# Kernel tuning notes

Measured on AMD Instinct MI355X. Metric: run time of the kernel, lower is better.

Reference implementation:

```python
import jax, jax.numpy as jnp
import numpy as np

B, L, WD = 4096, 30, 300          # batch of news, title length, word dim
H, AD = 20, 20                    # attention heads, per-head dim
MD = H * AD                       # multi_dim = 400
E, ED = 10, 100                   # entities per news, entity dim
QD = 200                          # query_vector_dim
CAT, CD = 18, 50                  # category vocab / dim
SUB, SD = 300, 50                 # subcategory vocab / dim


def _mha(x, wq, bq, wk, bk, wv, bv):
    # x: [B, L, Din] -> [B, L, MD]; standard multi-head self-attention
    b, l, _ = x.shape
    q = (x @ wq + bq).reshape(b, l, H, AD)
    k = (x @ wk + bk).reshape(b, l, H, AD)
    v = (x @ wv + bv).reshape(b, l, H, AD)
    scores = jnp.einsum('blhd,bmhd->bhlm', q, k) / jnp.sqrt(jnp.asarray(AD, x.dtype))
    attn = jax.nn.softmax(scores, axis=-1)
    out = jnp.einsum('bhlm,bmhd->blhd', attn, v)
    return out.reshape(b, l, MD)


def _layernorm(x, g, b):
    mu = jnp.mean(x, axis=-1, keepdims=True)
    var = jnp.var(x, axis=-1, keepdims=True)
    return (x - mu) / jnp.sqrt(var + 1e-5) * g + b


def _additive(x, w, b, q):
    # x: [B, L, D] -> [B, D]
    scores = jnp.tanh(x @ w + b) @ q            # [B, L]
    alpha = jax.nn.softmax(scores, axis=-1)
    return jnp.einsum('bl,bld->bd', alpha, x)


def setup_inputs() -> dict:
    key = jax.random.key(0)
    ks = iter(jax.random.split(key, 40))
    n = lambda shape, s=0.02: (jax.random.normal(next(ks), shape, dtype=jnp.float32) * s)
    inp = {
        'word_embedding': jax.random.normal(next(ks), (B, L, WD), dtype=jnp.float32),
        'entity_embedding': jax.random.normal(next(ks), (B, E, ED), dtype=jnp.float32),
        'category_index': jax.random.randint(next(ks), (B,), 0, CAT, dtype=jnp.int64 if jax.config.jax_enable_x64 else jnp.int32),
        'subcategory_index': jax.random.randint(next(ks), (B,), 0, SUB, dtype=jnp.int64 if jax.config.jax_enable_x64 else jnp.int32),
        # category / subcategory branches
        'emb_cat': n((CAT, CD), 1.0), 'fc1_w': n((CD, MD)), 'fc1_b': jnp.zeros((MD,), jnp.float32),
        'emb_sub': n((SUB, SD), 1.0), 'fc2_w': n((SD, MD)), 'fc2_b': jnp.zeros((MD,), jnp.float32),
        # word multi-head self-attention
        'wq': n((WD, MD)), 'bq': jnp.zeros((MD,), jnp.float32),
        'wk': n((WD, MD)), 'bk': jnp.zeros((MD,), jnp.float32),
        'wv': n((WD, MD)), 'bv': jnp.zeros((MD,), jnp.float32),
        # shared LayerNorm
        'ln_g': jnp.ones((MD,), jnp.float32), 'ln_b': jnp.zeros((MD,), jnp.float32),
        # word additive attention
        'wa_w': n((MD, QD)), 'wa_b': jnp.zeros((QD,), jnp.float32), 'wa_q': n((QD,), 1.0),
        # entity branch: fc3 + GCN (learnable adjacency over the E entities of a news)
        'fc3_w': n((ED, ED)), 'fc3_b': jnp.zeros((ED,), jnp.float32),
        'gcn_A': n((E, E), 1.0), 'gcn_w': n((ED, MD)), 'gcn_b': jnp.zeros((MD,), jnp.float32),
        'ea_w': n((MD, QD)), 'ea_b': jnp.zeros((QD,), jnp.float32), 'ea_q': n((QD,), 1.0),
        # final news-level additive attention over 4 views
        'na_w': n((MD, QD)), 'na_b': jnp.zeros((QD,), jnp.float32), 'na_q': n((QD,), 1.0),
    }
    return inp


def reference(word_embedding, entity_embedding, category_index, subcategory_index,
              emb_cat, fc1_w, fc1_b, emb_sub, fc2_w, fc2_b,
              wq, bq, wk, bk, wv, bv, ln_g, ln_b,
              wa_w, wa_b, wa_q, fc3_w, fc3_b, gcn_A, gcn_w, gcn_b,
              ea_w, ea_b, ea_q, na_w, na_b, na_q):
    # category / subcategory reps (dropout is identity in eval)
    cat_rep = jnp.tanh(emb_cat[category_index] @ fc1_w + fc1_b)      # [B, MD]
    sub_rep = jnp.tanh(emb_sub[subcategory_index] @ fc2_w + fc2_b)   # [B, MD]
    # word branch
    w = _mha(word_embedding, wq, bq, wk, bk, wv, bv)                 # [B, L, MD]
    w = _layernorm(w, ln_g, ln_b)
    word_rep = jnp.tanh(_additive(w, wa_w, wa_b, wa_q))              # [B, MD]
    # entity branch: fc3 -> intra-news GCN -> shared LayerNorm
    e = jnp.tanh(entity_embedding @ fc3_w + fc3_b)                   # [B, E, ED]
    e = jax.nn.relu(jnp.einsum('ef,bfd->bed', gcn_A, e) @ gcn_w + gcn_b)  # [B, E, MD]
    e = _layernorm(e, ln_g, ln_b)
    ent_rep = jnp.tanh(_additive(e, ea_w, ea_b, ea_q))               # [B, MD]
    # fuse the 4 views with additive attention
    views = jnp.stack([word_rep, ent_rep, cat_rep, sub_rep], axis=1)  # [B, 4, MD]
    news_rep = jnp.tanh(_additive(views, na_w, na_b, na_q))          # [B, MD]
    return news_rep
```

## Files before the change

kernel.cpp:

```cpp
#include <hip/hip_runtime.h>
#include <hip/hip_bf16.h>
#include <math.h>

#define B_  4096
#define L_  30
#define WD_ 300
#define H_  20
#define AD_ 20
#define MD_ 400
#define E_  10
#define ED_ 100
#define QD_ 200
#define CD_ 50
#define SD_ 50

typedef unsigned short ushort_t;
typedef __attribute__((ext_vector_type(8))) short bf16x8_t;
typedef __attribute__((ext_vector_type(4))) float f32x4_t;

#define SX_STR   328
#define QKV_STR  1218
#define OUTB_STR 424
#define SOUT_STR 401
#define P_STR    40
#define WT_K     320
#define WAT_K    416

#define N_WT    (1200 * WT_K)
#define N_WAT   (208 * WAT_K)
#define N_FC3T  (112 * 128)
#define N_GCNT  (400 * 128)
#define N_EAT   (208 * WAT_K)

union FragU {
  unsigned  u[4];
  short     s[8];
  bf16x8_t  h;
};

__device__ __forceinline__ ushort_t f2bf(float f) {
  unsigned u = __builtin_bit_cast(unsigned, f);
  unsigned r = (u + 0x7fffu + ((u >> 16) & 1u)) >> 16;
  return (ushort_t)r;
}
__device__ __forceinline__ float bf2f(ushort_t h) {
  return __builtin_bit_cast(float, ((unsigned)h) << 16);
}
__device__ __forceinline__ float wave_reduce_sum(float v) {
  #pragma unroll
  for (int off = 32; off > 0; off >>= 1) v += __shfl_xor(v, off);
  return v;
}
__device__ __forceinline__ void split2(float v, ushort_t* __restrict__ H,
                                       ushort_t* __restrict__ Lo, int idx) {
  const ushort_t h = f2bf(v);
  H[idx] = h;
  Lo[idx] = f2bf(v - bf2f(h));
}

__global__ __launch_bounds__(256) void prep_weights(
    const float* __restrict__ wq, const float* __restrict__ wk, const float* __restrict__ wv,
    const float* __restrict__ wa_w, const float* __restrict__ fc3_w,
    const float* __restrict__ gcn_w, const float* __restrict__ ea_w,
    ushort_t* __restrict__ Wt, ushort_t* __restrict__ Wat,
    ushort_t* __restrict__ fc3TH, ushort_t* __restrict__ fc3TL,
    ushort_t* __restrict__ gcnTH, ushort_t* __restrict__ gcnTL,
    ushort_t* __restrict__ eaTH, ushort_t* __restrict__ eaTL)
{
  int idx = blockIdx.x * 256 + threadIdx.x;
  if (idx < N_WT) {
    const int n = idx / WT_K, k = idx - n * WT_K;
    float v = 0.f;
    if (k < WD_) {
      const float* w = (n < 400) ? wq : (n < 800) ? wk : wv;
      const int c = (n < 400) ? n : (n < 800) ? n - 400 : n - 800;
      v = w[k * MD_ + c];
    }
    Wt[idx] = f2bf(v);
    return;
  }
  idx -= N_WT;
  if (idx < N_WAT) {
    const int q = idx / WAT_K, d = idx - q * WAT_K;
    Wat[idx] = (q < QD_ && d < MD_) ? f2bf(wa_w[d * QD_ + q]) : (ushort_t)0;
    return;
  }
  idx -= N_WAT;
  if (idx < N_FC3T) {
    const int n = idx / 128, k = idx - n * 128;
    const float v = (n < ED_ && k < ED_) ? fc3_w[k * ED_ + n] : 0.f;
    split2(v, fc3TH, fc3TL, idx);
    return;
  }
  idx -= N_FC3T;
  if (idx < N_GCNT) {
    const int n = idx / 128, k = idx - n * 128;
    const float v = (k < ED_) ? gcn_w[k * MD_ + n] : 0.f;
    split2(v, gcnTH, gcnTL, idx);
    return;
  }
  idx -= N_GCNT;
  if (idx < N_EAT) {
    const int q = idx / WAT_K, d = idx - q * WAT_K;
    const float v = (q < QD_ && d < MD_) ? ea_w[d * QD_ + q] : 0.f;
    split2(v, eaTH, eaTL, idx);
  }
}

__global__ __launch_bounds__(1024, 4) void word_branch_kernel(
    const float* __restrict__ X,
    const ushort_t* __restrict__ Wt, const ushort_t* __restrict__ Wat,
    const float* __restrict__ bq, const float* __restrict__ bk, const float* __restrict__ bv,
    const float* __restrict__ ln_g, const float* __restrict__ ln_b,
    const float* __restrict__ wa_b, const float* __restrict__ wa_q,
    float* __restrict__ word_rep)
{
  __shared__ __align__(16) union {
    ushort_t x[32 * SX_STR];
    ushort_t p[16 * 16 * P_STR];
  } uA;
  __shared__ __align__(16) union {
    ushort_t qkv[30 * QKV_STR];
    ushort_t o[32 * OUTB_STR];
  } uB;
  __shared__ __align__(16) float sOut[30 * SOUT_STR];
  __shared__ float sSc[32];
  __shared__ float sAlpha[32];

  const int b    = blockIdx.x;
  const int tid  = threadIdx.x;
  const int wave = tid >> 6;
  const int lane = tid & 63;
  const int lr   = lane & 15;
  const int kg   = lane >> 4;

  const float* xb = X + (size_t)b * (L_ * WD_);
  {
    const int r = tid >> 5;
    const int c0 = tid & 31;
    #pragma unroll
    for (int k = 0; k < 10; ++k) {
      const int c = c0 + k * 32;
      const float v = (r < L_ && c < WD_) ? xb[r * WD_ + c] : 0.f;
      uA.x[r * SX_STR + c] = f2bf(v);
    }
  }
  if (tid < 32) sSc[tid] = 0.f;
  __syncthreads();

  bf16x8_t axl[10], axh[10];
  #pragma unroll
  for (int ks = 0; ks < 10; ++ks) {
    axl[ks] = *reinterpret_cast<const bf16x8_t*>(&uA.x[lr * SX_STR + ks * 32 + kg * 8]);
    axh[ks] = *reinterpret_cast<const bf16x8_t*>(&uA.x[(16 + lr) * SX_STR + ks * 32 + kg * 8]);
  }
  for (int nt = wave; nt < 75; nt += 16) {
    const ushort_t* wbase = &Wt[(nt * 16 + lr) * WT_K + kg * 8];
    f32x4_t acc0 = {0,0,0,0}, acc1 = {0,0,0,0};
    #pragma unroll
    for (int ks = 0; ks < 10; ++ks) {
      bf16x8_t bf = *reinterpret_cast<const bf16x8_t*>(wbase + ks * 32);
      acc0 = __builtin_amdgcn_mfma_f32_16x16x32_bf16(axl[ks], bf, acc0, 0, 0, 0);
      acc1 = __builtin_amdgcn_mfma_f32_16x16x32_bf16(axh[ks], bf, acc1, 0, 0, 0);
    }
    const int col = nt * 16 + lr;
    const float bias = (col < 400) ? bq[col] : (col < 800) ? bk[col - 400] : bv[col - 800];
    #pragma unroll
    for (int i = 0; i < 4; ++i) {
      uB.qkv[(kg * 4 + i) * QKV_STR + col] = f2bf(acc0[i] + bias);
      const int r2 = 16 + kg * 4 + i;
      if (r2 < L_) uB.qkv[r2 * QKV_STR + col] = f2bf(acc1[i] + bias);
    }
  }
  __syncthreads();

  ushort_t* pw = &uA.p[wave * (16 * P_STR)];
  for (int u = wave; u < 2 * H_; u += 16) {
    const int h = u >> 1, mt = u & 1;
    const int hq = h * AD_, hk = 400 + h * AD_, hv = 800 + h * AD_;

    bf16x8_t aq, bkf[2];
    {
      FragU fq;
      fq.u[0]=fq.u[1]=fq.u[2]=fq.u[3]=0;
      const bool okrow = (mt == 0) || (lr < 14);
      if (okrow && kg < 3) {
        const ushort_t* pq = &uB.qkv[(mt * 16 + lr) * QKV_STR + hq + kg * 8];
        fq.u[0] = *(const unsigned*)(pq);     fq.u[1] = *(const unsigned*)(pq + 2);
        if (kg < 2) { fq.u[2] = *(const unsigned*)(pq + 4); fq.u[3] = *(const unsigned*)(pq + 6); }
      }
      aq = fq.h;
    }
    #pragma unroll
    for (int t = 0; t < 2; ++t) {
      FragU fk;
      fk.u[0]=fk.u[1]=fk.u[2]=fk.u[3]=0;
      const bool okrow = (t == 0) || (lr < 14);
      if (okrow && kg < 3) {
        const ushort_t* pk = &uB.qkv[(t * 16 + lr) * QKV_STR + hk + kg * 8];
        fk.u[0] = *(const unsigned*)(pk);     fk.u[1] = *(const unsigned*)(pk + 2);
        if (kg < 2) { fk.u[2] = *(const unsigned*)(pk + 4); fk.u[3] = *(const unsigned*)(pk + 6); }
      }
      bkf[t] = fk.h;
    }
    f32x4_t c0 = {0,0,0,0}, c1 = {0,0,0,0};
    c0 = __builtin_amdgcn_mfma_f32_16x16x32_bf16(aq, bkf[0], c0, 0, 0, 0);
    c1 = __builtin_amdgcn_mfma_f32_16x16x32_bf16(aq, bkf[1], c1, 0, 0, 0);

    const float SCALE = 0.2236067977499790f;
    #pragma unroll
    for (int i = 0; i < 4; ++i) {
      const float v0 = c0[i] * SCALE;
      const float v1 = (lr < 14) ? c1[i] * SCALE : -1e30f;
      float mx = fmaxf(v0, v1);
      mx = fmaxf(mx, __shfl_xor(mx, 1));
      mx = fmaxf(mx, __shfl_xor(mx, 2));
      mx = fmaxf(mx, __shfl_xor(mx, 4));
      mx = fmaxf(mx, __shfl_xor(mx, 8));
      const float e0 = __expf(v0 - mx);
      const float e1 = (lr < 14) ? __expf(v1 - mx) : 0.f;
      float s = e0 + e1;
      s += __shfl_xor(s, 1);
      s += __shfl_xor(s, 2);
      s += __shfl_xor(s, 4);
      s += __shfl_xor(s, 8);
      const float inv = 1.f / s;
      const int row = kg * 4 + i;
      pw[row * P_STR + lr]      = f2bf(e0 * inv);
      pw[row * P_STR + 16 + lr] = f2bf(e1 * inv);
    }
    __asm__ volatile("s_waitcnt lgkmcnt(0)" ::: "memory");

    bf16x8_t ap = *reinterpret_cast<const bf16x8_t*>(&pw[lr * P_STR + kg * 8]);
    bf16x8_t bvf[2];
    #pragma unroll
    for (int nt = 0; nt < 2; ++nt) {
      FragU f;
      const int d = nt * 16 + lr;
      if (d < AD_) {
        #pragma unroll
        for (int j = 0; j < 8; ++j) {
          const int rm = kg * 8 + j;
          f.s[j] = (rm < L_) ? (short)uB.qkv[rm * QKV_STR + hv + d] : (short)0;
        }
      } else {
        f.u[0]=f.u[1]=f.u[2]=f.u[3]=0;
      }
      bvf[nt] = f.h;
    }
    f32x4_t o0 = {0,0,0,0}, o1 = {0,0,0,0};
    o0 = __builtin_amdgcn_mfma_f32_16x16x32_bf16(ap, bvf[0], o0, 0, 0, 0);
    o1 = __builtin_amdgcn_mfma_f32_16x16x32_bf16(ap, bvf[1], o1, 0, 0, 0);

    #pragma unroll
    for (int nt = 0; nt < 2; ++nt) {
      const f32x4_t o = nt ? o1 : o0;
      const int d = nt * 16 + lr;
      if (d < AD_) {
        #pragma unroll
        for (int i = 0; i < 4; ++i) {
          const int r = mt * 16 + kg * 4 + i;
          if (r < L_) sOut[r * SOUT_STR + h * AD_ + d] = o[i];
        }
      }
    }
  }
  __syncthreads();

  for (int r = wave; r < L_; r += 16) {
    float s = 0.f, s2 = 0.f;
    for (int d = lane; d < MD_; d += 64) { const float v = sOut[r * SOUT_STR + d]; s += v; s2 += v * v; }
    s  = wave_reduce_sum(s);
    s2 = wave_reduce_sum(s2);
    const float mu  = s * (1.f / MD_);
    const float var = s2 * (1.f / MD_) - mu * mu;
    const float inv = rsqrtf(var + 1e-5f);
    for (int d = lane; d < MD_; d += 64) {
      const float nv = (sOut[r * SOUT_STR + d] - mu) * inv * ln_g[d] + ln_b[d];
      sOut[r * SOUT_STR + d] = nv;
      uB.o[r * OUTB_STR + d] = f2bf(nv);
    }
  }
  if (tid < 2 * 416) {
    const int r = 30 + (tid / 416), c = tid - (tid / 416) * 416;
    uB.o[r * OUTB_STR + c] = 0;
  }
  {
    const int id = tid;
    if (id < 30 * 16) {
      const int r = id >> 4, c = 400 + (id & 15);
      uB.o[r * OUTB_STR + c] = 0;
    }
  }
  __syncthreads();

  for (int t = wave; t < 26; t += 16) {
    const int mt = t & 1, nt = t >> 1;
    bf16x8_t afa[13];
    #pragma unroll
    for (int ks = 0; ks < 13; ++ks)
      afa[ks] = *reinterpret_cast<const bf16x8_t*>(&uB.o[(mt * 16 + lr) * OUTB_STR + ks * 32 + kg * 8]);
    const ushort_t* wbase = &Wat[(nt * 16 + lr) * WAT_K + kg * 8];
    f32x4_t acc = {0,0,0,0};
    #pragma unroll
    for (int ks = 0; ks < 13; ++ks) {
      bf16x8_t wf = *reinterpret_cast<const bf16x8_t*>(wbase + ks * 32);
      acc = __builtin_amdgcn_mfma_f32_16x16x32_bf16(afa[ks], wf, acc, 0, 0, 0);
    }
    const int q = nt * 16 + lr;
    if (q < QD_) {
      const float bb = wa_b[q], qq = wa_q[q];
      #pragma unroll
      for (int i = 0; i < 4; ++i) {
        const int row = mt * 16 + kg * 4 + i;
        if (row < L_) atomicAdd(&sSc[row], tanhf(acc[i] + bb) * qq);
      }
    }
  }
  __syncthreads();

  if (wave == 0) {
    const float v = (lane < L_) ? sSc[lane] : -1e30f;
    float mx = v;
    #pragma unroll
    for (int off = 32; off > 0; off >>= 1) mx = fmaxf(mx, __shfl_xor(mx, off));
    const float e = (lane < L_) ? __expf(v - mx) : 0.f;
    float s = e;
    #pragma unroll
    for (int off = 32; off > 0; off >>= 1) s += __shfl_xor(s, off);
    if (lane < L_) sAlpha[lane] = e / s;
  }
  __syncthreads();

  if (tid < MD_) {
    const int d = tid;
    float acc = 0.f;
    #pragma unroll 6
    for (int l = 0; l < L_; ++l) acc += sAlpha[l] * sOut[l * SOUT_STR + d];
    word_rep[(size_t)b * MD_ + d] = tanhf(acc);
  }
}

__global__ __launch_bounds__(512, 4) void entity_branch_kernel(
    const float* __restrict__ Ein,
    const ushort_t* __restrict__ fc3TH, const ushort_t* __restrict__ fc3TL,
    const float* __restrict__ fc3_b,
    const float* __restrict__ gcn_A,
    const ushort_t* __restrict__ gcnTH, const ushort_t* __restrict__ gcnTL,
    const float* __restrict__ gcn_b,
    const float* __restrict__ ln_g, const float* __restrict__ ln_b,
    const ushort_t* __restrict__ eaTH, const ushort_t* __restrict__ eaTL,
    const float* __restrict__ ea_b, const float* __restrict__ ea_q,
    float* __restrict__ ent_rep)
{
  __shared__ __align__(16) ushort_t sEh[16 * 136], sEl[16 * 136];
  __shared__ __align__(16) float    eF[E_ * 104];
  __shared__ __align__(16) ushort_t gH[16 * 136], gL[16 * 136];
  __shared__ __align__(16) float    sR[16 * SOUT_STR];
  __shared__ __align__(16) ushort_t oH[16 * OUTB_STR], oL[16 * OUTB_STR];
  __shared__ float sSc[16];
  __shared__ float sAlpha[16];

  const int b    = blockIdx.x;
  const int tid  = threadIdx.x;
  const int wave = tid >> 6;
  const int lane = tid & 63;
  const int lr   = lane & 15;
  const int kg   = lane >> 4;

  for (int id = tid; id < 16 * 128; id += 512) {
    const int r = id >> 7, c = id & 127;
    const float v = (r < E_ && c < ED_) ? Ein[(size_t)b * (E_ * ED_) + r * ED_ + c] : 0.f;
    const ushort_t hh = f2bf(v);
    sEh[r * 136 + c] = hh;
    sEl[r * 136 + c] = f2bf(v - bf2f(hh));
  }
  for (int id = tid; id < 16 * 136; id += 512) { gH[id] = 0; gL[id] = 0; }
  for (int id = tid; id < 16 * OUTB_STR; id += 512) { oH[id] = 0; oL[id] = 0; }
  if (tid < 16) sSc[tid] = 0.f;
  __syncthreads();

  for (int nt = wave; nt < 7; nt += 8) {
    f32x4_t acc = {0,0,0,0};
    #pragma unroll
    for (int ks = 0; ks < 4; ++ks) {
      const int kb = ks * 32 + kg * 8;
      bf16x8_t ah = *reinterpret_cast<const bf16x8_t*>(&sEh[lr * 136 + kb]);
      bf16x8_t al = *reinterpret_cast<const bf16x8_t*>(&sEl[lr * 136 + kb]);
      bf16x8_t wh = *reinterpret_cast<const bf16x8_t*>(&fc3TH[(nt * 16 + lr) * 128 + kb]);
      bf16x8_t wl = *reinterpret_cast<const bf16x8_t*>(&fc3TL[(nt * 16 + lr) * 128 + kb]);
      acc = __builtin_amdgcn_mfma_f32_16x16x32_bf16(ah, wh, acc, 0, 0, 0);
      acc = __builtin_amdgcn_mfma_f32_16x16x32_bf16(al, wh, acc, 0, 0, 0);
      acc = __builtin_amdgcn_mfma_f32_16x16x32_bf16(ah, wl, acc, 0, 0, 0);
    }
    const int d = nt * 16 + lr;
    if (d < ED_) {
      const float bias = fc3_b[d];
      #pragma unroll
      for (int i = 0; i < 4; ++i) {
        const int r = kg * 4 + i;
        if (r < E_) eF[r * 104 + d] = tanhf(acc[i] + bias);
      }
    }
  }
  __syncthreads();

  for (int id = tid; id < E_ * ED_; id += 512) {
    const int i = id / ED_, d = id - (id / ED_) * ED_;
    float acc = 0.f;
    #pragma unroll
    for (int f = 0; f < E_; ++f) acc += gcn_A[i * E_ + f] * eF[f * 104 + d];
    const ushort_t hh = f2bf(acc);
    gH[i * 136 + d] = hh;
    gL[i * 136 + d] = f2bf(acc - bf2f(hh));
  }
  __syncthreads();

  for (int nt = wave; nt < 25; nt += 8) {
    f32x4_t acc = {0,0,0,0};
    #pragma unroll
    for (int ks = 0; ks < 4; ++ks) {
      const int kb = ks * 32 + kg * 8;
// ... 119 lines not shown
  const int b = blockIdx.x, tid = threadIdx.x;
  for (int d = tid; d < MD_; d += 256) {
    sViews[0][d] = word_rep[(size_t)b * MD_ + d];
    sViews[1][d] = ent_rep[(size_t)b * MD_ + d];
    sViews[2][d] = cat_rep[(size_t)b * MD_ + d];
    sViews[3][d] = sub_rep[(size_t)b * MD_ + d];
  }
  if (tid < 4) sSc[tid] = 0.f;
  __syncthreads();
  for (int id = tid; id < 4 * QD_; id += 256) {
    const int v = id / QD_, q = id - (id / QD_) * QD_;
    float acc = na_b[q];
    #pragma unroll 4
    for (int d = 0; d < MD_; ++d) acc += sViews[v][d] * na_w[d * QD_ + q];
    atomicAdd(&sSc[v], tanhf(acc) * na_q[q]);
  }
  __syncthreads();
  if (tid == 0) {
    float mx = -1e30f;
    for (int v = 0; v < 4; ++v) mx = fmaxf(mx, sSc[v]);
    float sum = 0.f;
    for (int v = 0; v < 4; ++v) { const float e = __expf(sSc[v] - mx); sAlpha[v] = e; sum += e; }
    const float inv = 1.f / sum;
    for (int v = 0; v < 4; ++v) sAlpha[v] *= inv;
  }
  __syncthreads();
  for (int d = tid; d < MD_; d += 256) {
    const float acc = sAlpha[0] * sViews[0][d] + sAlpha[1] * sViews[1][d] +
                      sAlpha[2] * sViews[2][d] + sAlpha[3] * sViews[3][d];
    out[(size_t)b * MD_ + d] = tanhf(acc);
  }
}

extern "C" void kernel_launch(void* const* d_in, const int* in_sizes, int n_in,
                              void* d_out, int out_size, void* d_ws, size_t ws_size,
                              hipStream_t stream) {
  const float* X        = (const float*)d_in[0];
  const float* Ein      = (const float*)d_in[1];
  const int*   cat_idx  = (const int*)d_in[2];
  const int*   sub_idx  = (const int*)d_in[3];
  const float* emb_cat  = (const float*)d_in[4];
  const float* fc1_w    = (const float*)d_in[5];
  const float* fc1_b    = (const float*)d_in[6];
  const float* emb_sub  = (const float*)d_in[7];
  const float* fc2_w    = (const float*)d_in[8];
  const float* fc2_b    = (const float*)d_in[9];
  const float* wq       = (const float*)d_in[10];
  const float* bq       = (const float*)d_in[11];
  const float* wk       = (const float*)d_in[12];
  const float* bk       = (const float*)d_in[13];
  const float* wv       = (const float*)d_in[14];
  const float* bv       = (const float*)d_in[15];
  const float* ln_g     = (const float*)d_in[16];
  const float* ln_b     = (const float*)d_in[17];
  const float* wa_w     = (const float*)d_in[18];
  const float* wa_b     = (const float*)d_in[19];
  const float* wa_q     = (const float*)d_in[20];
  const float* fc3_w    = (const float*)d_in[21];
  const float* fc3_b    = (const float*)d_in[22];
  const float* gcn_A    = (const float*)d_in[23];
  const float* gcn_w    = (const float*)d_in[24];
  const float* gcn_b    = (const float*)d_in[25];
  const float* ea_w     = (const float*)d_in[26];
  const float* ea_b     = (const float*)d_in[27];
  const float* ea_q     = (const float*)d_in[28];
  const float* na_w     = (const float*)d_in[29];
  const float* na_b     = (const float*)d_in[30];
  const float* na_q     = (const float*)d_in[31];

  float* out = (float*)d_out;
  const size_t BM = (size_t)B_ * MD_;
  float* word_rep = (float*)d_ws;
  float* ent_rep  = word_rep + BM;
  float* cat_rep  = ent_rep + BM;
  float* sub_rep  = cat_rep + BM;
  ushort_t* Wt    = (ushort_t*)(sub_rep + BM);
  ushort_t* Wat   = Wt + N_WT;
  ushort_t* fc3TH = Wat + N_WAT;
  ushort_t* fc3TL = fc3TH + N_FC3T;
  ushort_t* gcnTH = fc3TL + N_FC3T;
  ushort_t* gcnTL = gcnTH + N_GCNT;
  ushort_t* eaTH  = gcnTL + N_GCNT;
  ushort_t* eaTL  = eaTH + N_EAT;

  {
    const int total = N_WT + N_WAT + N_FC3T + N_GCNT + N_EAT;
    prep_weights<<<(total + 255) / 256, 256, 0, stream>>>(
        wq, wk, wv, wa_w, fc3_w, gcn_w, ea_w,
        Wt, Wat, fc3TH, fc3TL, gcnTH, gcnTL, eaTH, eaTL);
  }
  word_branch_kernel<<<B_, 1024, 0, stream>>>(X, Wt, Wat, bq, bk, bv,
                                              ln_g, ln_b, wa_b, wa_q, word_rep);
  entity_branch_kernel<<<B_, 512, 0, stream>>>(Ein, fc3TH, fc3TL, fc3_b, gcn_A,
                                               gcnTH, gcnTL, gcn_b,
                                               ln_g, ln_b, eaTH, eaTL, ea_b, ea_q, ent_rep);
  catsub_kernel<<<(2 * B_ * MD_) / 256, 256, 0, stream>>>(cat_idx, sub_idx,
                                                          emb_cat, fc1_w, fc1_b,
                                                          emb_sub, fc2_w, fc2_b,
                                                          cat_rep, sub_rep);
  fuse_kernel<<<B_, 256, 0, stream>>>(word_rep, ent_rep, cat_rep, sub_rep,
                                      na_w, na_b, na_q, out);
}
```

Before: 1.312 ms.

## Make word-branch kernel persistent with half-width QKV staging and global MHA scratch

The word-branch kernel now runs as 512 persistent blocks of 512 threads, each looping over 8 news items instead of one 1024-thread block per item. QKV is computed and consumed in two passes of 10 heads each, so the shared staging buffer is halved. The fp32 attention output moves from shared memory to a per-block global scratch buffer. Together these cut shared-memory and thread footprint per block to raise residency, at the cost of extra global/L2 traffic for the MHA output and more barriers per item.

Result: slower. 1.448 ms (+10.3%).

```diff
diff --git a/kernel.cpp b/kernel.cpp
--- a/kernel.cpp
+++ b/kernel.cpp
@@ -18,13 +18,16 @@
 typedef __attribute__((ext_vector_type(8))) short bf16x8_t;
 typedef __attribute__((ext_vector_type(4))) float f32x4_t;
 
-#define SX_STR   328
-#define QKV_STR  1218
-#define OUTB_STR 424
-#define SOUT_STR 401
-#define P_STR    40
-#define WT_K     320
-#define WAT_K    416
+#define SX_STR    328
+#define QKVH_STR  626
+#define OUTB_STR  424
+#define SOUT_STR  401
+#define P_STR     40
+#define WT_K      320
+#define WAT_K     416
+
+#define WBLK      512
+#define ITERS     (B_ / WBLK)
 
 #define N_WT    (1200 * WT_K)
 #define N_WAT   (208 * WAT_K)
@@ -107,237 +110,262 @@
   }
 }
 
-__global__ __launch_bounds__(1024, 4) void word_branch_kernel(
+__global__ __launch_bounds__(512, 4) void word_branch_kernel(
     const float* __restrict__ X,
     const ushort_t* __restrict__ Wt, const ushort_t* __restrict__ Wat,
     const float* __restrict__ bq, const float* __restrict__ bk, const float* __restrict__ bv,
     const float* __restrict__ ln_g, const float* __restrict__ ln_b,
     const float* __restrict__ wa_b, const float* __restrict__ wa_q,
+    float* __restrict__ wsMha,
     float* __restrict__ word_rep)
 {
+  __shared__ __align__(16) ushort_t sX[32 * SX_STR];
   __shared__ __align__(16) union {
-    ushort_t x[32 * SX_STR];
-    ushort_t p[16 * 16 * P_STR];
-  } uA;
-  __shared__ __align__(16) union {
-    ushort_t qkv[30 * QKV_STR];
+    ushort_t qkv[30 * QKVH_STR];
     ushort_t o[32 * OUTB_STR];
   } uB;
-  __shared__ __align__(16) float sOut[30 * SOUT_STR];
+  __shared__ __align__(16) ushort_t pT[8 * 16 * P_STR];
   __shared__ float sSc[32];
   __shared__ float sAlpha[32];
 
-  const int b    = blockIdx.x;
   const int tid  = threadIdx.x;
   const int wave = tid >> 6;
   const int lane = tid & 63;
   const int lr   = lane & 15;
   const int kg   = lane >> 4;
-
-  const float* xb = X + (size_t)b * (L_ * WD_);
-  {
-    const int r = tid >> 5;
-    const int c0 = tid & 31;
-    #pragma unroll
-    for (int k = 0; k < 10; ++k) {
-      const int c = c0 + k * 32;
-      const float v = (r < L_ && c < WD_) ? xb[r * WD_ + c] : 0.f;
-      uA.x[r * SX_STR + c] = f2bf(v);
-    }
-  }
-  if (tid < 32) sSc[tid] = 0.f;
-  __syncthreads();
-
-  bf16x8_t axl[10], axh[10];
-  #pragma unroll
-  for (int ks = 0; ks < 10; ++ks) {
-    axl[ks] = *reinterpret_cast<const bf16x8_t*>(&uA.x[lr * SX_STR + ks * 32 + kg * 8]);
-    axh[ks] = *reinterpret_cast<const bf16x8_t*>(&uA.x[(16 + lr) * SX_STR + ks * 32 + kg * 8]);
-  }
-  for (int nt = wave; nt < 75; nt += 16) {
-    const ushort_t* wbase = &Wt[(nt * 16 + lr) * WT_K + kg * 8];
-    f32x4_t acc0 = {0,0,0,0}, acc1 = {0,0,0,0};
+  float* wsl = wsMha + (size_t)blockIdx.x * (30 * 400);
+  ushort_t* pw = &pT[wave * (16 * P_STR)];
+
+  for (int it = 0; it < ITERS; ++it) {
+    const int b = blockIdx.x + it * WBLK;
+
+    const float* xb = X + (size_t)b * (L_ * WD_);
+    {
+      const int r = tid >> 4, c0 = tid & 15;
+      #pragma unroll
+      for (int k = 0; k < 20; ++k) {
+        const int c = c0 + k * 16;
+        const float v = (r < L_ && c < WD_) ? xb[r * WD_ + c] : 0.f;
+        sX[r * SX_STR + c] = f2bf(v);
+      }
+    }
+    __syncthreads();
+
+    bf16x8_t axl[10], axh[10];
     #pragma unroll
     for (int ks = 0; ks < 10; ++ks) {
-      bf16x8_t bf = *reinterpret_cast<const bf16x8_t*>(wbase + ks * 32);
-      acc0 = __builtin_amdgcn_mfma_f32_16x16x32_bf16(axl[ks], bf, acc0, 0, 0, 0);
-      acc1 = __builtin_amdgcn_mfma_f32_16x16x32_bf16(axh[ks], bf, acc1, 0, 0, 0);
-    }
-    const int col = nt * 16 + lr;
-    const float bias = (col < 400) ? bq[col] : (col < 800) ? bk[col - 400] : bv[col - 800];
-    #pragma unroll
-    for (int i = 0; i < 4; ++i) {
-      uB.qkv[(kg * 4 + i) * QKV_STR + col] = f2bf(acc0[i] + bias);
-      const int r2 = 16 + kg * 4 + i;
-      if (r2 < L_) uB.qkv[r2 * QKV_STR + col] = f2bf(acc1[i] + bias);
-    }
-  }
-  __syncthreads();
-
-  ushort_t* pw = &uA.p[wave * (16 * P_STR)];
-  for (int u = wave; u < 2 * H_; u += 16) {
-    const int h = u >> 1, mt = u & 1;
-    const int hq = h * AD_, hk = 400 + h * AD_, hv = 800 + h * AD_;
-
-    bf16x8_t aq, bkf[2];
-    {
-      FragU fq;
-      fq.u[0]=fq.u[1]=fq.u[2]=fq.u[3]=0;
-      const bool okrow = (mt == 0) || (lr < 14);
-      if (okrow && kg < 3) {
-        const ushort_t* pq = &uB.qkv[(mt * 16 + lr) * QKV_STR + hq + kg * 8];
-        fq.u[0] = *(const unsigned*)(pq);     fq.u[1] = *(const unsigned*)(pq + 2);
-        if (kg < 2) { fq.u[2] = *(const unsigned*)(pq + 4); fq.u[3] = *(const unsigned*)(pq + 6); }
-      }
-      aq = fq.h;
-    }
-    #pragma unroll
-    for (int t = 0; t < 2; ++t) {
-      FragU fk;
-      fk.u[0]=fk.u[1]=fk.u[2]=fk.u[3]=0;
-      const bool okrow = (t == 0) || (lr < 14);
-      if (okrow && kg < 3) {
-        const ushort_t* pk = &uB.qkv[(t * 16 + lr) * QKV_STR + hk + kg * 8];
-        fk.u[0] = *(const unsigned*)(pk);     fk.u[1] = *(const unsigned*)(pk + 2);
-        if (kg < 2) { fk.u[2] = *(const unsigned*)(pk + 4); fk.u[3] = *(const unsigned*)(pk + 6); }
-      }
-      bkf[t] = fk.h;
-    }
-    f32x4_t c0 = {0,0,0,0}, c1 = {0,0,0,0};
-    c0 = __builtin_amdgcn_mfma_f32_16x16x32_bf16(aq, bkf[0], c0, 0, 0, 0);
-    c1 = __builtin_amdgcn_mfma_f32_16x16x32_bf16(aq, bkf[1], c1, 0, 0, 0);
-
-    const float SCALE = 0.2236067977499790f;
-    #pragma unroll
-    for (int i = 0; i < 4; ++i) {
-      const float v0 = c0[i] * SCALE;
-      const float v1 = (lr < 14) ? c1[i] * SCALE : -1e30f;
-      float mx = fmaxf(v0, v1);
-      mx = fmaxf(mx, __shfl_xor(mx, 1));
-      mx = fmaxf(mx, __shfl_xor(mx, 2));
-      mx = fmaxf(mx, __shfl_xor(mx, 4));
-      mx = fmaxf(mx, __shfl_xor(mx, 8));
-      const float e0 = __expf(v0 - mx);
-      const float e1 = (lr < 14) ? __expf(v1 - mx) : 0.f;
-      float s = e0 + e1;
-      s += __shfl_xor(s, 1);
-      s += __shfl_xor(s, 2);
-      s += __shfl_xor(s, 4);
-      s += __shfl_xor(s, 8);
-      const float inv = 1.f / s;
-      const int row = kg * 4 + i;
-      pw[row * P_STR + lr]      = f2bf(e0 * inv);
-      pw[row * P_STR + 16 + lr] = f2bf(e1 * inv);
-    }
-    __asm__ volatile("s_waitcnt lgkmcnt(0)" ::: "memory");
-
-    bf16x8_t ap = *reinterpret_cast<const bf16x8_t*>(&pw[lr * P_STR + kg * 8]);
-    bf16x8_t bvf[2];
-    #pragma unroll
-    for (int nt = 0; nt < 2; ++nt) {
-      FragU f;
-      const int d = nt * 16 + lr;
-      if (d < AD_) {
+      axl[ks] = *reinterpret_cast<const bf16x8_t*>(&sX[lr * SX_STR + ks * 32 + kg * 8]);
+      axh[ks] = *reinterpret_cast<const bf16x8_t*>(&sX[(16 + lr) * SX_STR + ks * 32 + kg * 8]);
+    }
+
+    #pragma unroll 1
+    for (int pass = 0; pass < 2; ++pass) {
+      const int qg  = pass ? 192 : 0;
+      const int kgb = pass ? 592 : 400;
+      const int vg  = pass ? 992 : 800;
+
+      for (int t = wave; t < 39; t += 8) {
+        const int sect = t / 13, ti = t - sect * 13;
+        const int gbase = ((sect == 0) ? qg : (sect == 1) ? kgb : vg) + ti * 16;
+        const int n = gbase + lr;
+        const ushort_t* wbase = &Wt[n * WT_K + kg * 8];
+        f32x4_t acc0 = {0,0,0,0}, acc1 = {0,0,0,0};
         #pragma unroll
-        for (int j = 0; j < 8; ++j) {
-          const int rm = kg * 8 + j;
-          f.s[j] = (rm < L_) ? (short)uB.qkv[rm * QKV_STR + hv + d] : (short)0;
-        }
-      } else {
-        f.u[0]=f.u[1]=f.u[2]=f.u[3]=0;
-      }
-      bvf[nt] = f.h;
-    }
-    f32x4_t o0 = {0,0,0,0}, o1 = {0,0,0,0};
-    o0 = __builtin_amdgcn_mfma_f32_16x16x32_bf16(ap, bvf[0], o0, 0, 0, 0);
-    o1 = __builtin_amdgcn_mfma_f32_16x16x32_bf16(ap, bvf[1], o1, 0, 0, 0);
-
-    #pragma unroll
-    for (int nt = 0; nt < 2; ++nt) {
-      const f32x4_t o = nt ? o1 : o0;
-      const int d = nt * 16 + lr;
-      if (d < AD_) {
+        for (int ks = 0; ks < 10; ++ks) {
+          bf16x8_t bf = *reinterpret_cast<const bf16x8_t*>(wbase + ks * 32);
+          acc0 = __builtin_amdgcn_mfma_f32_16x16x32_bf16(axl[ks], bf, acc0, 0, 0, 0);
+          acc1 = __builtin_amdgcn_mfma_f32_16x16x32_bf16(axh[ks], bf, acc1, 0, 0, 0);
+        }
+        const float bias = (n < 400) ? bq[n] : (n < 800) ? bk[n - 400] : bv[n - 800];
+        const int lcol = sect * 208 + ti * 16 + lr;
         #pragma unroll
         for (int i = 0; i < 4; ++i) {
-          const int r = mt * 16 + kg * 4 + i;
-          if (r < L_) sOut[r * SOUT_STR + h * AD_ + d] = o[i];
-        }
-      }
-    }
-  }
-  __syncthreads();
-
-  for (int r = wave; r < L_; r += 16) {
-    float s = 0.f, s2 = 0.f;
-    for (int d = lane; d < MD_; d += 64) { const float v = sOut[r * SOUT_STR + d]; s += v; s2 += v * v; }
-    s  = wave_reduce_sum(s);
-    s2 = wave_reduce_sum(s2);
-    const float mu  = s * (1.f / MD_);
-    const float var = s2 * (1.f / MD_) - mu * mu;
-    const float inv = rsqrtf(var + 1e-5f);
-    for (int d = lane; d < MD_; d += 64) {
-      const float nv = (sOut[r * SOUT_STR + d] - mu) * inv * ln_g[d] + ln_b[d];
-      sOut[r * SOUT_STR + d] = nv;
-      uB.o[r * OUTB_STR + d] = f2bf(nv);
-    }
-  }
-  if (tid < 2 * 416) {
-    const int r = 30 + (tid / 416), c = tid - (tid / 416) * 416;
-    uB.o[r * OUTB_STR + c] = 0;
-  }
-  {
-    const int id = tid;
-    if (id < 30 * 16) {
+          uB.qkv[(kg * 4 + i) * QKVH_STR + lcol] = f2bf(acc0[i] + bias);
+          const int r2 = 16 + kg * 4 + i;
+          if (r2 < L_) uB.qkv[r2 * QKVH_STR + lcol] = f2bf(acc1[i] + bias);
+        }
+      }
+      __syncthreads();
+
+      for (int u = wave; u < 20; u += 8) {
+        const int hl = u >> 1, mt = u & 1;
+        const int h = pass * 10 + hl;
+        const int qloc = h * 20 - qg;
+        const int kloc = 208 + (400 + h * 20 - kgb);
+        const int vloc = 416 + (800 + h * 20 - vg);
+
+        bf16x8_t aq, bkf[2];
+        {
+          FragU fq;
+          fq.u[0]=fq.u[1]=fq.u[2]=fq.u[3]=0;
+          const bool okrow = (mt == 0) || (lr < 14);
+          if (okrow && kg < 3) {
+            const ushort_t* pq = &uB.qkv[(mt * 16 + lr) * QKVH_STR + qloc + kg * 8];
+            fq.u[0] = *(const unsigned*)(pq);     fq.u[1] = *(const unsigned*)(pq + 2);
+            if (kg < 2) { fq.u[2] = *(const unsigned*)(pq + 4); fq.u[3] = *(const unsigned*)(pq + 6); }
+          }
+          aq = fq.h;
+        }
+        #pragma unroll
+        for (int t = 0; t < 2; ++t) {
+          FragU fk;
+          fk.u[0]=fk.u[1]=fk.u[2]=fk.u[3]=0;
+          const bool okrow = (t == 0) || (lr < 14);
+          if (okrow && kg < 3) {
+            const ushort_t* pk = &uB.qkv[(t * 16 + lr) * QKVH_STR + kloc + kg * 8];
+            fk.u[0] = *(const unsigned*)(pk);     fk.u[1] = *(const unsigned*)(pk + 2);
+            if (kg < 2) { fk.u[2] = *(const unsigned*)(pk + 4); fk.u[3] = *(const unsigned*)(pk + 6); }
+          }
+          bkf[t] = fk.h;
+        }
+        f32x4_t c0 = {0,0,0,0}, c1 = {0,0,0,0};
+        c0 = __builtin_amdgcn_mfma_f32_16x16x32_bf16(aq, bkf[0], c0, 0, 0, 0);
+        c1 = __builtin_amdgcn_mfma_f32_16x16x32_bf16(aq, bkf[1], c1, 0, 0, 0);
+
+        const float SCALE = 0.2236067977499790f;
+        #pragma unroll
+        for (int i = 0; i < 4; ++i) {
+          const float v0 = c0[i] * SCALE;
+          const float v1 = (lr < 14) ? c1[i] * SCALE : -1e30f;
+          float mx = fmaxf(v0, v1);
+          mx = fmaxf(mx, __shfl_xor(mx, 1));
+          mx = fmaxf(mx, __shfl_xor(mx, 2));
+          mx = fmaxf(mx, __shfl_xor(mx, 4));
+          mx = fmaxf(mx, __shfl_xor(mx, 8));
+          const float e0 = __expf(v0 - mx);
+          const float e1 = (lr < 14) ? __expf(v1 - mx) : 0.f;
+          float s = e0 + e1;
+          s += __shfl_xor(s, 1);
+          s += __shfl_xor(s, 2);
+          s += __shfl_xor(s, 4);
+          s += __shfl_xor(s, 8);
+          const float inv = 1.f / s;
+          const int row = kg * 4 + i;
+          pw[row * P_STR + lr]      = f2bf(e0 * inv);
+          pw[row * P_STR + 16 + lr] = f2bf(e1 * inv);
+        }
+        __asm__ volatile("s_waitcnt lgkmcnt(0)" ::: "memory");
+
+        bf16x8_t ap = *reinterpret_cast<const bf16x8_t*>(&pw[lr * P_STR + kg * 8]);
+        bf16x8_t bvf[2];
+        #pragma unroll
+        for (int nt = 0; nt < 2; ++nt) {
+          FragU f;
+          const int d = nt * 16 + lr;
+          if (d < AD_) {
+            #pragma unroll
+            for (int j = 0; j < 8; ++j) {
+              const int rm = kg * 8 + j;
+              f.s[j] = (rm < L_) ? (short)uB.qkv[rm * QKVH_STR + vloc + d] : (short)0;
+            }
+          } else {
+            f.u[0]=f.u[1]=f.u[2]=f.u[3]=0;
+          }
+          bvf[nt] = f.h;
+        }
+        f32x4_t o0 = {0,0,0,0}, o1 = {0,0,0,0};
+        o0 = __builtin_amdgcn_mfma_f32_16x16x32_bf16(ap, bvf[0], o0, 0, 0, 0);
+        o1 = __builtin_amdgcn_mfma_f32_16x16x32_bf16(ap, bvf[1], o1, 0, 0, 0);
+
+        #pragma unroll
+        for (int nt = 0; nt < 2; ++nt) {
+          const f32x4_t o = nt ? o1 : o0;
+          const int d = nt * 16 + lr;
+          if (d < AD_) {
+            #pragma unroll
+            for (int i = 0; i < 4; ++i) {
+              const int r = mt * 16 + kg * 4 + i;
+              if (r < L_) wsl[r * 400 + h * AD_ + d] = o[i];
+            }
+          }
+        }
+      }
+      __syncthreads();
+    }
+
+    __threadfence_block();
+    __syncthreads();
+
+    for (int r = wave; r < L_; r += 8) {
+      float s = 0.f, s2 = 0.f;
+      #pragma unroll
+      for (int j = 0; j < 7; ++j) {
+        const int d = lane + j * 64;
+        if (d < MD_) { const float v = wsl[r * 400 + d]; s += v; s2 += v * v; }
+      }
+      s  = wave_reduce_sum(s);
+      s2 = wave_reduce_sum(s2);
+      const float mu  = s * (1.f / MD_);
+      const float var = s2 * (1.f / MD_) - mu * mu;
+      const float inv = rsqrtf(var + 1e-5f);
+      #pragma unroll
+      for (int j = 0; j < 7; ++j) {
+        const int d = lane + j * 64;
+        if (d < MD_) {
+          const float nv = (wsl[r * 400 + d] - mu) * inv * ln_g[d] + ln_b[d];
+          wsl[r * 400 + d] = nv;
+          uB.o[r * OUTB_STR + d] = f2bf(nv);
+        }
+      }
+    }
+    for (int id = tid; id < 2 * 416; id += 512) {
+      const int r = 30 + id / 416, c = id - (id / 416) * 416;
+      uB.o[r * OUTB_STR + c] = 0;
+    }
+    for (int id = tid; id < 30 * 16; id += 512) {
       const int r = id >> 4, c = 400 + (id & 15);
       uB.o[r * OUTB_STR + c] = 0;
     }
-  }
-  __syncthreads();
-
-  for (int t = wave; t < 26; t += 16) {
-    const int mt = t & 1, nt = t >> 1;
-    bf16x8_t afa[13];
-    #pragma unroll
-    for (int ks = 0; ks < 13; ++ks)
-      afa[ks] = *reinterpret_cast<const bf16x8_t*>(&uB.o[(mt * 16 + lr) * OUTB_STR + ks * 32 + kg * 8]);
-    const ushort_t* wbase = &Wat[(nt * 16 + lr) * WAT_K + kg * 8];
-    f32x4_t acc = {0,0,0,0};
-    #pragma unroll
-    for (int ks = 0; ks < 13; ++ks) {
-      bf16x8_t wf = *reinterpret_cast<const bf16x8_t*>(wbase + ks * 32);
-      acc = __builtin_amdgcn_mfma_f32_16x16x32_bf16(afa[ks], wf, acc, 0, 0, 0);
-    }
-    const int q = nt * 16 + lr;
-    if (q < QD_) {
-      const float bb = wa_b[q], qq = wa_q[q];
-      #pragma unroll
-      for (int i = 0; i < 4; ++i) {
-        const int row = mt * 16 + kg * 4 + i;
-        if (row < L_) atomicAdd(&sSc[row], tanhf(acc[i] + bb) * qq);
-      }
-    }
-  }
-  __syncthreads();
-
-  if (wave == 0) {
-    const float v = (lane < L_) ? sSc[lane] : -1e30f;
-    float mx = v;
-    #pragma unroll
-    for (int off = 32; off > 0; off >>= 1) mx = fmaxf(mx, __shfl_xor(mx, off));
-    const float e = (lane < L_) ? __expf(v - mx) : 0.f;
-    float s = e;
-    #pragma unroll
-    for (int off = 32; off > 0; off >>= 1) s += __shfl_xor(s, off);
-    if (lane < L_) sAlpha[lane] = e / s;
-  }
-  __syncthreads();
-
-  if (tid < MD_) {
-    const int d = tid;
-    float acc = 0.f;
-    #pragma unroll 6
-    for (int l = 0; l < L_; ++l) acc += sAlpha[l] * sOut[l * SOUT_STR + d];
-    word_rep[(size_t)b * MD_ + d] = tanhf(acc);
+    if (tid < 32) sSc[tid] = 0.f;
+    __threadfence_block();
+    __syncthreads();
+
+    for (int t = wave; t < 26; t += 8) {
+      const int mt = t & 1, nt = t >> 1;
+      bf16x8_t afa[13];
+      #pragma unroll
+      for (int ks = 0; ks < 13; ++ks)
+        afa[ks] = *reinterpret_cast<const bf16x8_t*>(&uB.o[(mt * 16 + lr) * OUTB_STR + ks * 32 + kg * 8]);
+      const ushort_t* wbase = &Wat[(nt * 16 + lr) * WAT_K + kg * 8];
+      f32x4_t acc = {0,0,0,0};
+      #pragma unroll
+      for (int ks = 0; ks < 13; ++ks) {
+        bf16x8_t wf = *reinterpret_cast<const bf16x8_t*>(wbase + ks * 32);
+        acc = __builtin_amdgcn_mfma_f32_16x16x32_bf16(afa[ks], wf, acc, 0, 0, 0);
+      }
+      const int q = nt * 16 + lr;
+      if (q < QD_) {
+        const float bb = wa_b[q], qq = wa_q[q];
+        #pragma unroll
+        for (int i = 0; i < 4; ++i) {
+          const int row = mt * 16 + kg * 4 + i;
+          if (row < L_) atomicAdd(&sSc[row], tanhf(acc[i] + bb) * qq);
+        }
+      }
+    }
+    __syncthreads();
+
+    if (wave == 0) {
+      const float v = (lane < L_) ? sSc[lane] : -1e30f;
+      float mx = v;
+      #pragma unroll
+      for (int off = 32; off > 0; off >>= 1) mx = fmaxf(mx, __shfl_xor(mx, off));
+      const float e = (lane < L_) ? __expf(v - mx) : 0.f;
+      float s = e;
+      #pragma unroll
+      for (int off = 32; off > 0; off >>= 1) s += __shfl_xor(s, off);
+      if (lane < L_) sAlpha[lane] = e / s;
+    }
+    __syncthreads();
+
+    if (tid < MD_) {
+      const int d = tid;
+      float acc = 0.f;
+      #pragma unroll 6
+      for (int l = 0; l < L_; ++l) acc += sAlpha[l] * wsl[l * 400 + d];
+      word_rep[(size_t)b * MD_ + d] = tanhf(acc);
+    }
+    __syncthreads();
   }
 }
 
@@ -623,6 +651,7 @@
   ushort_t* gcnTL = gcnTH + N_GCNT;
   ushort_t* eaTH  = gcnTL + N_GCNT;
   ushort_t* eaTL  = eaTH + N_EAT;
+  float* wsMha    = (float*)(eaTL + N_EAT);
 
   {
     const int total = N_WT + N_WAT + N_FC3T + N_GCNT + N_EAT;
@@ -630,8 +659,9 @@
         wq, wk, wv, wa_w, fc3_w, gcn_w, ea_w,
         Wt, Wat, fc3TH, fc3TL, gcnTH, gcnTL, eaTH, eaTL);
   }
-  word_branch_kernel<<<B_, 1024, 0, stream>>>(X, Wt, Wat, bq, bk, bv,
-                                              ln_g, ln_b, wa_b, wa_q, word_rep);
+  word_branch_kernel<<<WBLK, 512, 0, stream>>>(X, Wt, Wat, bq, bk, bv,
+                                               ln_g, ln_b, wa_b, wa_q,
+                                               wsMha, word_rep);
   entity_branch_kernel<<<B_, 512, 0, stream>>>(Ein, fc3TH, fc3TL, fc3_b, gcn_A,
                                                gcnTH, gcnTL, gcn_b,
                                                ln_g, ln_b, eaTH, eaTL, ea_b, ea_q, ent_rep);
```

## Split fused word branch into batched QKV GEMM, attention, and tail kernels

Applied to the files above, without the earlier changes.

Replaces the single per-news 1024-thread word-branch kernel with three kernels: a QKV GEMM over 64-row tiles spanning many news items, a per-head attention kernel, and a layernorm plus additive-attention tail kernel. Intermediates go through workspace in chunks sized to the available workspace. The aim is to reuse the projection weights across more rows, cut per-block shared-memory pressure, and raise occupancy. In exchange it adds global-memory round trips for the QKV (bf16) and MHA (fp32) intermediates plus extra launches, and falls back to the fused kernel when workspace is too small.

Result: slower. 1.966 ms (+49.8%).

```diff
diff --git a/kernel.cpp b/kernel.cpp
--- a/kernel.cpp
+++ b/kernel.cpp
@@ -18,13 +18,13 @@
 typedef __attribute__((ext_vector_type(8))) short bf16x8_t;
 typedef __attribute__((ext_vector_type(4))) float f32x4_t;
 
-#define SX_STR   328
-#define QKV_STR  1218
-#define OUTB_STR 424
-#define SOUT_STR 401
-#define P_STR    40
-#define WT_K     320
-#define WAT_K    416
+#define SX_STR    328
+#define QKV_STR   1218
+#define OUTB_STR  424
+#define SOUT_STR  401
+#define P_STR     40
+#define WT_K      320
+#define WAT_K     416
 
 #define N_WT    (1200 * WT_K)
 #define N_WAT   (208 * WAT_K)
@@ -107,7 +107,258 @@
   }
 }
 
-__global__ __launch_bounds__(1024, 4) void word_branch_kernel(
+__global__ __launch_bounds__(512, 4) void qkv_gemm_kernel(
+    const float* __restrict__ X,
+    const ushort_t* __restrict__ Wt,
+    const float* __restrict__ bq, const float* __restrict__ bk, const float* __restrict__ bv,
+    ushort_t* __restrict__ qkvOut)
+{
+  __shared__ __align__(16) ushort_t sX[64 * SX_STR];
+  const int tid = threadIdx.x;
+  const int wave = tid >> 6, lane = tid & 63;
+  const int lr = lane & 15, kg = lane >> 4;
+  const int rbase = blockIdx.x * 64;
+
+  for (int idx = tid; idx < 64 * 320; idx += 512) {
+    const int r = idx / 320, c = idx - r * 320;
+    const float v = (c < WD_) ? X[(size_t)(rbase + r) * WD_ + c] : 0.f;
+    sX[r * SX_STR + c] = f2bf(v);
+  }
+  __syncthreads();
+
+  for (int nt = wave; nt < 75; nt += 8) {
+    const ushort_t* wbase = &Wt[(nt * 16 + lr) * WT_K + kg * 8];
+    bf16x8_t bfa[10];
+    #pragma unroll
+    for (int ks = 0; ks < 10; ++ks)
+      bfa[ks] = *reinterpret_cast<const bf16x8_t*>(wbase + ks * 32);
+    const int col = nt * 16 + lr;
+    const float bias = (col < 400) ? bq[col] : (col < 800) ? bk[col - 400] : bv[col - 800];
+    #pragma unroll
+    for (int ms = 0; ms < 4; ++ms) {
+      f32x4_t acc = {0,0,0,0};
+      #pragma unroll
+      for (int ks = 0; ks < 10; ++ks) {
+        bf16x8_t a = *reinterpret_cast<const bf16x8_t*>(&sX[(ms * 16 + lr) * SX_STR + ks * 32 + kg * 8]);
+        acc = __builtin_amdgcn_mfma_f32_16x16x32_bf16(a, bfa[ks], acc, 0, 0, 0);
+      }
+      #pragma unroll
+      for (int i = 0; i < 4; ++i)
+        qkvOut[(size_t)(rbase + ms * 16 + kg * 4 + i) * 1200 + col] = f2bf(acc[i] + bias);
+    }
+  }
+}
+
+__global__ __launch_bounds__(256, 4) void attn_kernel(
+    const ushort_t* __restrict__ qkv,
+    float* __restrict__ mha)
+{
+  __shared__ __align__(16) ushort_t pT[4 * 32 * P_STR];
+  const int tid = threadIdx.x;
+  const int wave = tid >> 6, lane = tid & 63;
+  const int lr = lane & 15, kg = lane >> 4;
+  const int bi = blockIdx.x / 5;
+  const int h  = (blockIdx.x - bi * 5) * 4 + wave;
+  const ushort_t* slab = qkv + (size_t)bi * (30 * 1200);
+  float* oslab = mha + (size_t)bi * (30 * 400);
+  ushort_t* pw = &pT[wave * (32 * P_STR)];
+  const int hq = h * AD_, hk = 400 + h * AD_, hv = 800 + h * AD_;
+
+  bf16x8_t aq[2], bkf[2];
+  #pragma unroll
+  for (int t = 0; t < 2; ++t) {
+    FragU fq, fk;
+    fq.u[0]=fq.u[1]=fq.u[2]=fq.u[3]=0;
+    fk.u[0]=fk.u[1]=fk.u[2]=fk.u[3]=0;
+    const bool okrow = (t == 0) || (lr < 14);
+    if (okrow && kg < 3) {
+      const ushort_t* pq = slab + (t * 16 + lr) * 1200 + hq + kg * 8;
+      const ushort_t* pk = slab + (t * 16 + lr) * 1200 + hk + kg * 8;
+      fq.u[0] = *(const unsigned*)(pq);     fq.u[1] = *(const unsigned*)(pq + 2);
+      fk.u[0] = *(const unsigned*)(pk);     fk.u[1] = *(const unsigned*)(pk + 2);
+      if (kg < 2) {
+        fq.u[2] = *(const unsigned*)(pq + 4); fq.u[3] = *(const unsigned*)(pq + 6);
+        fk.u[2] = *(const unsigned*)(pk + 4); fk.u[3] = *(const unsigned*)(pk + 6);
+      }
+    }
+    aq[t] = fq.h; bkf[t] = fk.h;
+  }
+  f32x4_t c00 = {0,0,0,0}, c01 = {0,0,0,0}, c10 = {0,0,0,0}, c11 = {0,0,0,0};
+  c00 = __builtin_amdgcn_mfma_f32_16x16x32_bf16(aq[0], bkf[0], c00, 0, 0, 0);
+  c01 = __builtin_amdgcn_mfma_f32_16x16x32_bf16(aq[0], bkf[1], c01, 0, 0, 0);
+  c10 = __builtin_amdgcn_mfma_f32_16x16x32_bf16(aq[1], bkf[0], c10, 0, 0, 0);
+  c11 = __builtin_amdgcn_mfma_f32_16x16x32_bf16(aq[1], bkf[1], c11, 0, 0, 0);
+
+  const float SCALE = 0.2236067977499790f;
+  #pragma unroll
+  for (int mt = 0; mt < 2; ++mt) {
+    const f32x4_t v0f = mt ? c10 : c00;
+    const f32x4_t v1f = mt ? c11 : c01;
+    #pragma unroll
+    for (int i = 0; i < 4; ++i) {
+      const float v0 = v0f[i] * SCALE;
+      const float v1 = (lr < 14) ? v1f[i] * SCALE : -1e30f;
+      float mx = fmaxf(v0, v1);
+      mx = fmaxf(mx, __shfl_xor(mx, 1));
+      mx = fmaxf(mx, __shfl_xor(mx, 2));
+      mx = fmaxf(mx, __shfl_xor(mx, 4));
+      mx = fmaxf(mx, __shfl_xor(mx, 8));
+      const float e0 = __expf(v0 - mx);
+      const float e1 = (lr < 14) ? __expf(v1 - mx) : 0.f;
+      float s = e0 + e1;
+      s += __shfl_xor(s, 1);
+      s += __shfl_xor(s, 2);
+      s += __shfl_xor(s, 4);
+      s += __shfl_xor(s, 8);
+      const float inv = 1.f / s;
+      const int row = mt * 16 + kg * 4 + i;
+      pw[row * P_STR + lr]      = f2bf(e0 * inv);
+      pw[row * P_STR + 16 + lr] = f2bf(e1 * inv);
+    }
+  }
+  __asm__ volatile("s_waitcnt lgkmcnt(0)" ::: "memory");
+  __builtin_amdgcn_sched_barrier(0);
+
+  bf16x8_t ap[2];
+  ap[0] = *reinterpret_cast<const bf16x8_t*>(&pw[lr * P_STR + kg * 8]);
+  ap[1] = *reinterpret_cast<const bf16x8_t*>(&pw[(16 + lr) * P_STR + kg * 8]);
+  bf16x8_t bvf[2];
+  #pragma unroll
+  for (int nt = 0; nt < 2; ++nt) {
+    FragU f;
+    const int d = nt * 16 + lr;
+    if (d < AD_) {
+      #pragma unroll
+      for (int j = 0; j < 8; ++j) {
+        const int rm = kg * 8 + j;
+        f.s[j] = (rm < L_) ? (short)slab[rm * 1200 + hv + d] : (short)0;
+      }
+    } else {
+      f.u[0]=f.u[1]=f.u[2]=f.u[3]=0;
+    }
+    bvf[nt] = f.h;
+  }
+  f32x4_t o0 = {0,0,0,0}, o1 = {0,0,0,0}, o2 = {0,0,0,0}, o3 = {0,0,0,0};
+  o0 = __builtin_amdgcn_mfma_f32_16x16x32_bf16(ap[0], bvf[0], o0, 0, 0, 0);
+  o1 = __builtin_amdgcn_mfma_f32_16x16x32_bf16(ap[0], bvf[1], o1, 0, 0, 0);
+  o2 = __builtin_amdgcn_mfma_f32_16x16x32_bf16(ap[1], bvf[0], o2, 0, 0, 0);
+  o3 = __builtin_amdgcn_mfma_f32_16x16x32_bf16(ap[1], bvf[1], o3, 0, 0, 0);
+
+  #pragma unroll
+  for (int mt = 0; mt < 2; ++mt) {
+    #pragma unroll
+    for (int nt = 0; nt < 2; ++nt) {
+      const f32x4_t o = mt ? (nt ? o3 : o2) : (nt ? o1 : o0);
+      const int d = nt * 16 + lr;
+      if (d < AD_) {
+        #pragma unroll
+        for (int i = 0; i < 4; ++i) {
+          const int r = mt * 16 + kg * 4 + i;
+          if (r < L_) oslab[r * 400 + h * AD_ + d] = o[i];
+        }
+      }
+    }
+  }
+}
+
+__global__ __launch_bounds__(256, 4) void word_tail_kernel(
+    float* __restrict__ mha,
+    const ushort_t* __restrict__ Wat,
+    const float* __restrict__ ln_g, const float* __restrict__ ln_b,
+    const float* __restrict__ wa_b, const float* __restrict__ wa_q,
+    float* __restrict__ word_rep, int c0)
+{
+  __shared__ __align__(16) ushort_t o[32 * OUTB_STR];
+  __shared__ float sSc[32];
+  __shared__ float sAlpha[32];
+  const int tid = threadIdx.x;
+  const int wave = tid >> 6, lane = tid & 63;
+  const int lr = lane & 15, kg = lane >> 4;
+  const int bi = blockIdx.x;
+  float* slab = mha + (size_t)bi * (30 * 400);
+
+  for (int id = tid; id < 2 * 416; id += 256) {
+    const int r = 30 + id / 416, c = id - (id / 416) * 416;
+    o[r * OUTB_STR + c] = 0;
+  }
+  for (int id = tid; id < 30 * 16; id += 256) {
+    const int r = id >> 4, c = 400 + (id & 15);
+    o[r * OUTB_STR + c] = 0;
+  }
+  if (tid < 32) sSc[tid] = 0.f;
+
+  for (int r = wave; r < L_; r += 4) {
+    float s = 0.f, s2 = 0.f;
+    #pragma unroll
+    for (int j = 0; j < 7; ++j) {
+      const int d = lane + j * 64;
+      if (d < MD_) { const float v = slab[r * 400 + d]; s += v; s2 += v * v; }
+    }
+    s  = wave_reduce_sum(s);
+    s2 = wave_reduce_sum(s2);
+    const float mu  = s * (1.f / MD_);
+    const float var = s2 * (1.f / MD_) - mu * mu;
+    const float inv = rsqrtf(var + 1e-5f);
+    #pragma unroll
+    for (int j = 0; j < 7; ++j) {
+      const int d = lane + j * 64;
+      if (d < MD_) {
+        const float nv = (slab[r * 400 + d] - mu) * inv * ln_g[d] + ln_b[d];
+        slab[r * 400 + d] = nv;
+        o[r * OUTB_STR + d] = f2bf(nv);
+      }
+    }
+  }
+  __threadfence_block();
+  __syncthreads();
+
+  for (int t = wave; t < 26; t += 4) {
+    const int mt = t & 1, nt = t >> 1;
+    bf16x8_t afa[13];
+    #pragma unroll
+    for (int ks = 0; ks < 13; ++ks)
+      afa[ks] = *reinterpret_cast<const bf16x8_t*>(&o[(mt * 16 + lr) * OUTB_STR + ks * 32 + kg * 8]);
+    const ushort_t* wbase = &Wat[(nt * 16 + lr) * WAT_K + kg * 8];
+    f32x4_t acc = {0,0,0,0};
+    #pragma unroll
+    for (int ks = 0; ks < 13; ++ks) {
+      bf16x8_t wf = *reinterpret_cast<const bf16x8_t*>(wbase + ks * 32);
+      acc = __builtin_amdgcn_mfma_f32_16x16x32_bf16(afa[ks], wf, acc, 0, 0, 0);
+    }
+    const int q = nt * 16 + lr;
+    if (q < QD_) {
+      const float bb = wa_b[q], qq = wa_q[q];
+      #pragma unroll
+      for (int i = 0; i < 4; ++i) {
+        const int row = mt * 16 + kg * 4 + i;
+        if (row < L_) atomicAdd(&sSc[row], tanhf(acc[i] + bb) * qq);
+      }
+    }
+  }
+  __syncthreads();
+
+  if (wave == 0) {
+    const float v = (lane < L_) ? sSc[lane] : -1e30f;
+    float mx = v;
+    #pragma unroll
+    for (int off = 32; off > 0; off >>= 1) mx = fmaxf(mx, __shfl_xor(mx, off));
+    const float e = (lane < L_) ? __expf(v - mx) : 0.f;
+    float s = e;
+    #pragma unroll
+    for (int off = 32; off > 0; off >>= 1) s += __shfl_xor(s, off);
+    if (lane < L_) sAlpha[lane] = e / s;
+  }
+  __syncthreads();
+
+  for (int d = tid; d < MD_; d += 256) {
+    float acc = 0.f;
+    #pragma unroll 6
+    for (int l = 0; l < L_; ++l) acc += sAlpha[l] * slab[l * 400 + d];
+    word_rep[(size_t)(c0 + bi) * MD_ + d] = tanhf(acc);
+  }
+}
+
+__global__ __launch_bounds__(1024, 4) void word_branch_fused(
     const float* __restrict__ X,
     const ushort_t* __restrict__ Wt, const ushort_t* __restrict__ Wat,
     const float* __restrict__ bq, const float* __restrict__ bk, const float* __restrict__ bv,
@@ -623,6 +874,20 @@
   ushort_t* gcnTL = gcnTH + N_GCNT;
   ushort_t* eaTH  = gcnTL + N_GCNT;
   ushort_t* eaTL  = eaTH + N_EAT;
+  char* wsFree    = (char*)(eaTL + N_EAT);
+  size_t baseBytes = (size_t)(wsFree - (char*)d_ws);
+  size_t off = (baseBytes + 255) & ~(size_t)255;
+
+  int C = 0;
+  const int cands[6] = {4096, 2048, 1024, 512, 256, 128};
+  size_t qkvOff = 0, mhaOff = 0;
+  for (int ci = 0; ci < 6; ++ci) {
+    const int cc = cands[ci];
+    size_t qo = off;
+    size_t mo = (qo + (size_t)cc * 72000 + 255) & ~(size_t)255;
+    size_t end = mo + (size_t)cc * 48000;
+    if (end <= ws_size) { C = cc; qkvOff = qo; mhaOff = mo; break; }
+  }
 
   {
     const int total = N_WT + N_WAT + N_FC3T + N_GCNT + N_EAT;
@@ -630,8 +895,22 @@
         wq, wk, wv, wa_w, fc3_w, gcn_w, ea_w,
         Wt, Wat, fc3TH, fc3TL, gcnTH, gcnTL, eaTH, eaTL);
   }
-  word_branch_kernel<<<B_, 1024, 0, stream>>>(X, Wt, Wat, bq, bk, bv,
-                                              ln_g, ln_b, wa_b, wa_q, word_rep);
+
+  if (C > 0) {
+    ushort_t* wsQKV = (ushort_t*)((char*)d_ws + qkvOff);
+    float*    wsMHA = (float*)((char*)d_ws + mhaOff);
+    for (int c0 = 0; c0 < B_; c0 += C) {
+      qkv_gemm_kernel<<<(C * 30) / 64, 512, 0, stream>>>(
+          X + (size_t)c0 * (L_ * WD_), Wt, bq, bk, bv, wsQKV);
+      attn_kernel<<<C * 5, 256, 0, stream>>>(wsQKV, wsMHA);
+      word_tail_kernel<<<C, 256, 0, stream>>>(wsMHA, Wat, ln_g, ln_b,
+                                              wa_b, wa_q, word_rep, c0);
+    }
+  } else {
+    word_branch_fused<<<B_, 1024, 0, stream>>>(X, Wt, Wat, bq, bk, bv,
+                                               ln_g, ln_b, wa_b, wa_q, word_rep);
+  }
+
   entity_branch_kernel<<<B_, 512, 0, stream>>>(Ein, fc3TH, fc3TL, fc3_b, gcn_A,
                                                gcnTH, gcnTL, gcn_b,
                                                ln_g, ln_b, eaTH, eaTL, ea_b, ea_q, ent_rep);
```
